# Performance work log

Hardware: AMD Instinct MI355X
Metric: run time of the kernel (lower is better)

The kernel has to match this reference:

```python
import jax, jax.numpy as jnp
import numpy as np

IN_F = 4096
OUT_F = 4096

def setup_inputs() -> dict:
    key = jax.random.key(0)
    k1, k2 = jax.random.split(key)
    x = jax.random.normal(k1, (4, 2048, IN_F), dtype=jnp.float32)
    W = jax.random.normal(k2, (OUT_F, IN_F), dtype=jnp.float32) * (1.0 / np.sqrt(IN_F))
    return {"x": x, "W": W}

def reference(x, W):
    # per-tensor scale = mean |W|, clamped
    scale = jnp.maximum(jnp.mean(jnp.abs(W)), 1e-8)
    # pentanet: 5-level quantization {-2,-1,0,1,2}
    w_quant = jnp.clip(jnp.round(W / scale), -2.0, 2.0)
    # STE: forward uses quantized weights, gradient flows to W
    w_ste = jax.lax.stop_gradient(w_quant * scale - W) + W
    # F.linear: x @ w_ste.T -> [b, s, out]
    return jnp.einsum('bsi,oi->bso', x, w_ste)
```

## Files before the change

kernel.cpp:

```cpp
#include <hip/hip_runtime.h>
#include <cstdint>
#include <cstddef>

#define IN_F 4096
#define OUT_F 4096

typedef __attribute__((ext_vector_type(8))) short bf16x8;
typedef __attribute__((ext_vector_type(4))) float f32x4;

__device__ __forceinline__ ushort f32_bf16_rne(float f) {
    uint32_t u = __builtin_bit_cast(uint32_t, f);
    uint32_t r = (u + 0x7FFFu + ((u >> 16) & 1u)) >> 16;
    return (ushort)r;
}

__device__ __forceinline__ void gload_lds16(const void* g, void* l) {
    __builtin_amdgcn_global_load_lds(
        (const __attribute__((address_space(1))) uint32_t*)g,
        (__attribute__((address_space(3))) uint32_t*)l,
        16, 0, 0);
}

__device__ __forceinline__ void bar() {
    asm volatile("s_barrier" ::: "memory");
}

__global__ void reduce_abs1(const float* __restrict__ W, float* __restrict__ part) {
    __shared__ float sm[256];
    const int b = blockIdx.x, t = threadIdx.x;
    const float* p = W + (size_t)b * 4096;
    float s = 0.f;
#pragma unroll
    for (int j = 0; j < 16; ++j) s += fabsf(p[t + 256 * j]);
    sm[t] = s;
    __syncthreads();
    for (int w = 128; w > 0; w >>= 1) {
        if (t < w) sm[t] += sm[t + w];
        __syncthreads();
    }
    if (t == 0) part[b] = sm[0];
}

__global__ void reduce_abs2(const float* __restrict__ part, float* __restrict__ scale) {
    __shared__ float sm[256];
    const int t = threadIdx.x;
    float s = 0.f;
#pragma unroll
    for (int j = 0; j < 16; ++j) s += part[t + 256 * j];
    sm[t] = s;
    __syncthreads();
    for (int w = 128; w > 0; w >>= 1) {
        if (t < w) sm[t] += sm[t + w];
        __syncthreads();
    }
    if (t == 0) {
        float m = sm[0] / 16777216.0f;
        *scale = fmaxf(m, 1e-8f);
    }
}

__global__ void quantize_w(const float* __restrict__ W, ushort* __restrict__ wq,
                           const float* __restrict__ scale_p) {
    const int i = blockIdx.x * 256 + threadIdx.x;
    const float s = *scale_p;
    float4 v = ((const float4*)W)[i];
    float q0 = fminf(fmaxf(rintf(v.x / s), -2.f), 2.f);
    float q1 = fminf(fmaxf(rintf(v.y / s), -2.f), 2.f);
    float q2 = fminf(fmaxf(rintf(v.z / s), -2.f), 2.f);
    float q3 = fminf(fmaxf(rintf(v.w / s), -2.f), 2.f);
    ushort4 o;
    o.x = f32_bf16_rne(q0); o.y = f32_bf16_rne(q1);
    o.z = f32_bf16_rne(q2); o.w = f32_bf16_rne(q3);
    ((ushort4*)wq)[i] = o;
}

__global__ void cast_x(const float* __restrict__ X, ushort* __restrict__ xh) {
    const int i = blockIdx.x * 256 + threadIdx.x;
    float4 v = ((const float4*)X)[i];
    ushort4 o;
    o.x = f32_bf16_rne(v.x); o.y = f32_bf16_rne(v.y);
    o.z = f32_bf16_rne(v.z); o.w = f32_bf16_rne(v.w);
    ((ushort4*)xh)[i] = o;
}

#define BK 64
#define BUF_BYTES 65536

__global__ __launch_bounds__(512, 2) void qgemm256(
        const ushort* __restrict__ Ab, const ushort* __restrict__ Bq,
        float* __restrict__ C, const float* __restrict__ scale_p,
        int M, int N, int K) {
    extern __shared__ __align__(16) char smem[];

    const int t = threadIdx.x;
    const int lane = t & 63;
    const int w = t >> 6;
    const int wr = w >> 2;
    const int wc = w & 3;
    const int bh = wc >> 1;

    const int MT = M >> 8;
    const int NTiles = N >> 8;
    int mt, nt;
    if (MT == 32 && NTiles == 16 && gridDim.x == 512) {
        const int x = blockIdx.x & 7;
        const int j = blockIdx.x >> 3;
        const int jr = j & 31;
        const int r = j >> 5;
        mt = (x & 3) * 8 + (jr & 7);
        nt = r * 8 + (x >> 2) * 4 + (jr >> 3);
    } else {
        const int nwg = gridDim.x;
        int wg = blockIdx.x;
        if ((nwg & 7) == 0) wg = (wg & 7) * (nwg >> 3) + (wg >> 3);
        mt = wg % MT; nt = wg / MT;
    }
    const int m0 = mt << 8;
    const int n0 = nt << 8;

    const int NT = K / BK;

    int pre[2];
#pragma unroll
    for (int ks = 0; ks < 2; ++ks)
        pre[ks] = (lane & 15) * 128 +
                  (((ks * 64) + ((lane >> 4) * 16)) ^ ((lane & 7) << 4));

    const int rowA = t >> 3;
    const int colsw = ((t & 7) ^ ((t >> 3) & 7)) << 3;
    const ushort* gA0 = Ab + (size_t)(m0 + rowA) * K + colsw;
    const ushort* gA1 = Ab + (size_t)(m0 + 128 + rowA) * K + colsw;
    const ushort* gB0 = Bq + (size_t)(n0 + rowA) * K + colsw;
    const ushort* gB1 = Bq + (size_t)(n0 + 128 + rowA) * K + colsw;
    const size_t jrow = (size_t)64 * K;
    char* lb = smem + t * 16;

    auto stA = [&](uint32_t par) {
        gload_lds16(gA0,        lb + par);
        gload_lds16(gA0 + jrow, lb + par + 8192);
        gload_lds16(gA1,        lb + par + 16384);
        gload_lds16(gA1 + jrow, lb + par + 24576);
        gA0 += 64; gA1 += 64;
    };
    auto stB = [&](uint32_t par) {
        gload_lds16(gB0,        lb + par + 32768);
        gload_lds16(gB0 + jrow, lb + par + 40960);
        gload_lds16(gB1,        lb + par + 49152);
        gload_lds16(gB1 + jrow, lb + par + 57344);
        gB0 += 64; gB1 += 64;
    };

    const char* aBbase = smem + wr * 16384;
    const char* bBbase = smem + 32768 + bh * 16384 + (wc & 1) * 8192;

    f32x4 acc[8][4];
#pragma unroll
    for (int m = 0; m < 8; ++m)
#pragma unroll
        for (int n = 0; n < 4; ++n) acc[m][n] = (f32x4){0.f, 0.f, 0.f, 0.f};

    bf16x8 a0[4][2], a1[4][2], b01[2][2], b23[2][2];

    stA(0); stB(0);
    stA(BUF_BYTES); stB(BUF_BYTES);
    asm volatile("s_waitcnt vmcnt(8)" ::: "memory");
    bar();
#pragma unroll
    for (int m = 0; m < 4; ++m)
#pragma unroll
        for (int ks = 0; ks < 2; ++ks) {
            a0[m][ks] = *(const bf16x8*)(aBbase + m * 2048 + pre[ks]);
            a1[m][ks] = *(const bf16x8*)(aBbase + (m + 4) * 2048 + pre[ks]);
        }
#pragma unroll
    for (int n = 0; n < 2; ++n)
#pragma unroll
        for (int ks = 0; ks < 2; ++ks) {
            b01[n][ks] = *(const bf16x8*)(bBbase + n * 2048 + pre[ks]);
            b23[n][ks] = *(const bf16x8*)(bBbase + (n + 2) * 2048 + pre[ks]);
        }

    for (int kt = 0; kt < NT; ++kt) {
        const uint32_t cur = (uint32_t)(kt & 1) * BUF_BYTES;
        const uint32_t nxt = cur ^ BUF_BYTES;
        const char* aBn = aBbase + nxt;
        const char* bBn = bBbase + nxt;

        asm volatile("s_waitcnt vmcnt(0)" ::: "memory");
        if (kt + 2 < NT) { stA(cur); stB(cur); }
        bar();

        __builtin_amdgcn_s_setprio(1);
#pragma unroll
        for (int m = 0; m < 4; ++m)
#pragma unroll
            for (int n = 0; n < 2; ++n)
#pragma unroll
                for (int ks = 0; ks < 2; ++ks)
                    acc[m][n] = __builtin_amdgcn_mfma_f32_16x16x32_bf16(
                        a0[m][ks], b01[n][ks], acc[m][n], 0, 0, 0);
#pragma unroll
        for (int m = 0; m < 4; ++m)
#pragma unroll
            for (int n = 0; n < 2; ++n)
#pragma unroll
                for (int ks = 0; ks < 2; ++ks)
                    acc[m + 4][n] = __builtin_amdgcn_mfma_f32_16x16x32_bf16(
                        a1[m][ks], b01[n][ks], acc[m + 4][n], 0, 0, 0);
#pragma unroll
        for (int m = 0; m < 4; ++m)
#pragma unroll
            for (int n = 0; n < 2; ++n)
#pragma unroll
                for (int ks = 0; ks < 2; ++ks)
                    acc[m][n + 2] = __builtin_amdgcn_mfma_f32_16x16x32_bf16(
                        a0[m][ks], b23[n][ks], acc[m][n + 2], 0, 0, 0);
#pragma unroll
        for (int m = 0; m < 4; ++m)
#pragma unroll
            for (int n = 0; n < 2; ++n)
#pragma unroll
                for (int ks = 0; ks < 2; ++ks)
                    acc[m + 4][n + 2] = __builtin_amdgcn_mfma_f32_16x16x32_bf16(
                        a1[m][ks], b23[n][ks], acc[m + 4][n + 2], 0, 0, 0);
        if (kt + 1 < NT) {
#pragma unroll
            for (int m = 0; m < 4; ++m)
#pragma unroll
                for (int ks = 0; ks < 2; ++ks) {
                    a0[m][ks] = *(const bf16x8*)(aBn + m * 2048 + pre[ks]);
                    a1[m][ks] = *(const bf16x8*)(aBn + (m + 4) * 2048 + pre[ks]);
                }
#pragma unroll
            for (int n = 0; n < 2; ++n)
#pragma unroll
                for (int ks = 0; ks < 2; ++ks) {
                    b01[n][ks] = *(const bf16x8*)(bBn + n * 2048 + pre[ks]);
                    b23[n][ks] = *(const bf16x8*)(bBn + (n + 2) * 2048 + pre[ks]);
                }
        }
        __builtin_amdgcn_s_setprio(0);
        asm volatile("s_waitcnt lgkmcnt(0)" ::: "memory");
        bar();
    }

    const float s = *scale_p;
#pragma unroll
    for (int m = 0; m < 8; ++m)
#pragma unroll
        for (int n = 0; n < 4; ++n) {
            const int col = n0 + wc * 64 + n * 16 + (lane & 15);
            const int rbase = m0 + wr * 128 + m * 16 + ((lane >> 4) << 2);
#pragma unroll
            for (int j = 0; j < 4; ++j)
                C[(size_t)(rbase + j) * N + col] = s * acc[m][n][j];
        }
}

template <bool ABF16>
__global__ __launch_bounds__(256) void qgemm(const void* __restrict__ Aptr,
                                             const ushort* __restrict__ Bq,
                                             float* __restrict__ C,
                                             const float* __restrict__ scale_p,
                                             int M, int N, int K) {
    __shared__ __align__(16) ushort sA[128 * 64];
    __shared__ __align__(16) ushort sB[128 * 64];

    const int t = threadIdx.x;
    const int lane = t & 63;
    const int w = t >> 6;
    const int wr = w >> 1, wc = w & 1;

    const int nwg = gridDim.x;
    int wg = blockIdx.x;
    if ((nwg & 7) == 0) wg = (wg & 7) * (nwg >> 3) + (wg >> 3);
    const int MT = M >> 7;
    const int mt = wg % MT;
    const int nt = wg / MT;
    const int m0 = mt * 128, n0 = nt * 128;

    const ushort* Ab = (const ushort*)Aptr;
    const float* Af = (const float*)Aptr;

    f32x4 zero = {0.f, 0.f, 0.f, 0.f};
    f32x4 acc[4][4];
#pragma unroll
    for (int m = 0; m < 4; ++m)
#pragma unroll
        for (int n = 0; n < 4; ++n) acc[m][n] = zero;

    for (int k0 = 0; k0 < K; k0 += 64) {
#pragma unroll
        for (int i = 0; i < 4; ++i) {
            int e = i * 2048 + t * 8;
            int r = e >> 6, c8 = (e >> 3) & 7;
            int srcc = (c8 ^ (r & 7)) * 8;
            gload_lds16(Bq + (size_t)(n0 + r) * K + (k0 + srcc), &sB[e]);
        }
        if constexpr (ABF16) {
#pragma unroll
            for (int i = 0; i < 4; ++i) {
                int e = i * 2048 + t * 8;
                int r = e >> 6, c8 = (e >> 3) & 7;
                int srcc = (c8 ^ (r & 7)) * 8;
                gload_lds16(Ab + (size_t)(m0 + r) * K + (k0 + srcc), &sA[e]);
            }
        } else {
#pragma unroll
            for (int i = 0; i < 4; ++i) {
                int e = i * 2048 + t * 8;
                int r = e >> 6, c = e & 63;
                const float* src = Af + (size_t)(m0 + r) * K + (k0 + c);
                float4 v0 = *(const float4*)src;
                float4 v1 = *(const float4*)(src + 4);
                bf16x8 pk;
                pk[0] = (short)f32_bf16_rne(v0.x); pk[1] = (short)f32_bf16_rne(v0.y);
                pk[2] = (short)f32_bf16_rne(v0.z); pk[3] = (short)f32_bf16_rne(v0.w);
                pk[4] = (short)f32_bf16_rne(v1.x); pk[5] = (short)f32_bf16_rne(v1.y);
                pk[6] = (short)f32_bf16_rne(v1.z); pk[7] = (short)f32_bf16_rne(v1.w);
                int byte = (r * 128 + c * 2) ^ ((r & 7) << 4);
                *(bf16x8*)((char*)sA + byte) = pk;
            }
        }
        __syncthreads();

#pragma unroll
        for (int ks = 0; ks < 2; ++ks) {
            const int kk = ks * 32 + ((lane >> 4) << 3);
            bf16x8 afr[4], bfr[4];
#pragma unroll
            for (int m = 0; m < 4; ++m) {
                int r = wr * 64 + m * 16 + (lane & 15);
                int byte = (r * 128 + kk * 2) ^ ((r & 7) << 4);
                afr[m] = *(const bf16x8*)((const char*)sA + byte);
            }
#pragma unroll
            for (int n = 0; n < 4; ++n) {
                int r = wc * 64 + n * 16 + (lane & 15);
                int byte = (r * 128 + kk * 2) ^ ((r & 7) << 4);
                bfr[n] = *(const bf16x8*)((const char*)sB + byte);
            }
#pragma unroll
            for (int m = 0; m < 4; ++m)
#pragma unroll
                for (int n = 0; n < 4; ++n)
                    acc[m][n] = __builtin_amdgcn_mfma_f32_16x16x32_bf16(
                        afr[m], bfr[n], acc[m][n], 0, 0, 0);
        }
        __syncthreads();
    }

    const float s = *scale_p;
#pragma unroll
    for (int m = 0; m < 4; ++m)
#pragma unroll
        for (int n = 0; n < 4; ++n) {
            const int col = n0 + wc * 64 + n * 16 + (lane & 15);
            const int rbase = m0 + wr * 64 + m * 16 + ((lane >> 4) << 2);
#pragma unroll
            for (int j = 0; j < 4; ++j)
                C[(size_t)(rbase + j) * N + col] = s * acc[m][n][j];
        }
}

__global__ void naive_qgemm(const float* __restrict__ X, const float* __restrict__ W,
                            float* __restrict__ out, const float* __restrict__ scale_p,
                            int M) {
    const int col = blockIdx.x * 256 + threadIdx.x;
    const int row = blockIdx.y;
    const float s = *scale_p;
    const float inv = 1.0f / s;
    const float* xr = X + (size_t)row * IN_F;
    const float* wrow = W + (size_t)col * IN_F;
    float acc = 0.f;
    for (int k = 0; k < IN_F; ++k) {
        float q = fminf(fmaxf(rintf(wrow[k] * inv), -2.f), 2.f);
        acc += xr[k] * q;
    }
    out[(size_t)row * OUT_F + col] = acc * s;
}

extern "C" void kernel_launch(void* const* d_in, const int* in_sizes, int n_in,
                              void* d_out, int out_size, void* d_ws, size_t ws_size,
                              hipStream_t stream) {
    const float* x = (const float*)d_in[0];
    const float* W = (const float*)d_in[1];
    float* out = (float*)d_out;
    const int M = in_sizes[0] / IN_F;
    const int K = IN_F, N = OUT_F;

    char* ws = (char*)d_ws;
    const size_t OFF_PART = 512;
    const size_t OFF_WQ = OFF_PART + 4096 * sizeof(float);
    const size_t WQ_BYTES = (size_t)N * K * sizeof(ushort);
    const size_t OFF_XH = OFF_WQ + WQ_BYTES;
    const size_t XH_BYTES = (size_t)M * K * sizeof(ushort);
    float* scale = (float*)(ws + 0);
    float* part = (float*)(ws + OFF_PART);
    ushort* wq = (ushort*)(ws + OFF_WQ);
    ushort* xh = (ushort*)(ws + OFF_XH);

    if (ws_size < OFF_WQ) return;

    reduce_abs1<<<4096, 256, 0, stream>>>(W, part);
    reduce_abs2<<<1, 256, 0, stream>>>(part, scale);

    if (ws_size >= OFF_XH + XH_BYTES && (M % 256) == 0 && (N % 256) == 0) {
        quantize_w<<<(N * K / 4) / 256, 256, 0, stream>>>(W, wq, scale);
        cast_x<<<(M * K / 4) / 256, 256, 0, stream>>>(x, xh);
        (void)hipFuncSetAttribute((const void*)qgemm256,
                                  hipFuncAttributeMaxDynamicSharedMemorySize,
                                  131072);
        qgemm256<<<(M / 256) * (N / 256), 512, 131072, stream>>>(
            xh, wq, out, scale, M, N, K);
    } else if (ws_size >= OFF_XH + XH_BYTES) {
        quantize_w<<<(N * K / 4) / 256, 256, 0, stream>>>(W, wq, scale);
        cast_x<<<(M * K / 4) / 256, 256, 0, stream>>>(x, xh);
        qgemm<true><<<(M / 128) * (N / 128), 256, 0, stream>>>(xh, wq, out, scale, M, N, K);
    } else if (ws_size >= OFF_WQ + WQ_BYTES) {
        quantize_w<<<(N * K / 4) / 256, 256, 0, stream>>>(W, wq, scale);
        qgemm<false><<<(M / 128) * (N / 128), 256, 0, stream>>>(x, wq, out, scale, M, N, K);
    } else {
        naive_qgemm<<<dim3(N / 256, M), 256, 0, stream>>>(x, W, out, scale, M);
    }
}
```

Before: 313.9 us.

## Drop register prefetch and issue one-ahead global loads per K-step

Restructures the main loop pipeline. Before, the kernel loaded two LDS stages ahead and prefetched the next tile's fragments into registers after the MFMAs. Now each iteration issues the global-to-LDS load for the next stage only, waits on the current one, then reads fragments from LDS and runs the MFMAs. This cuts register pressure and simplifies the schedule, but LDS read latency is no longer hidden behind MFMAs and global prefetch depth shrinks from two stages to one.

```diff
diff --git a/kernel.cpp b/kernel.cpp
--- a/kernel.cpp
+++ b/kernel.cpp
@@ -159,38 +159,37 @@
 #pragma unroll
         for (int n = 0; n < 4; ++n) acc[m][n] = (f32x4){0.f, 0.f, 0.f, 0.f};
 
-    bf16x8 a0[4][2], a1[4][2], b01[2][2], b23[2][2];
-
     stA(0); stB(0);
-    stA(BUF_BYTES); stB(BUF_BYTES);
-    asm volatile("s_waitcnt vmcnt(8)" ::: "memory");
-    bar();
-#pragma unroll
-    for (int m = 0; m < 4; ++m)
-#pragma unroll
-        for (int ks = 0; ks < 2; ++ks) {
-            a0[m][ks] = *(const bf16x8*)(aBbase + m * 2048 + pre[ks]);
-            a1[m][ks] = *(const bf16x8*)(aBbase + (m + 4) * 2048 + pre[ks]);
-        }
-#pragma unroll
-    for (int n = 0; n < 2; ++n)
-#pragma unroll
-        for (int ks = 0; ks < 2; ++ks) {
-            b01[n][ks] = *(const bf16x8*)(bBbase + n * 2048 + pre[ks]);
-            b23[n][ks] = *(const bf16x8*)(bBbase + (n + 2) * 2048 + pre[ks]);
-        }
 
     for (int kt = 0; kt < NT; ++kt) {
         const uint32_t cur = (uint32_t)(kt & 1) * BUF_BYTES;
-        const uint32_t nxt = cur ^ BUF_BYTES;
-        const char* aBn = aBbase + nxt;
-        const char* bBn = bBbase + nxt;
-
-        asm volatile("s_waitcnt vmcnt(0)" ::: "memory");
-        if (kt + 2 < NT) { stA(cur); stB(cur); }
+        const char* aB = aBbase + cur;
+        const char* bB = bBbase + cur;
+
+        if (kt + 1 < NT) {
+            stA(cur ^ BUF_BYTES); stB(cur ^ BUF_BYTES);
+            asm volatile("s_waitcnt vmcnt(8)" ::: "memory");
+        } else {
+            asm volatile("s_waitcnt vmcnt(0)" ::: "memory");
+        }
         bar();
 
         __builtin_amdgcn_s_setprio(1);
+        bf16x8 a0[4][2], a1[4][2], b01[2][2], b23[2][2];
+#pragma unroll
+        for (int n = 0; n < 2; ++n)
+#pragma unroll
+            for (int ks = 0; ks < 2; ++ks) {
+                b01[n][ks] = *(const bf16x8*)(bB + n * 2048 + pre[ks]);
+                b23[n][ks] = *(const bf16x8*)(bB + (n + 2) * 2048 + pre[ks]);
+            }
+#pragma unroll
+        for (int m = 0; m < 4; ++m)
+#pragma unroll
+            for (int ks = 0; ks < 2; ++ks) {
+                a0[m][ks] = *(const bf16x8*)(aB + m * 2048 + pre[ks]);
+                a1[m][ks] = *(const bf16x8*)(aB + (m + 4) * 2048 + pre[ks]);
+            }
 #pragma unroll
         for (int m = 0; m < 4; ++m)
 #pragma unroll
@@ -223,22 +222,6 @@
                 for (int ks = 0; ks < 2; ++ks)
                     acc[m + 4][n + 2] = __builtin_amdgcn_mfma_f32_16x16x32_bf16(
                         a1[m][ks], b23[n][ks], acc[m + 4][n + 2], 0, 0, 0);
-        if (kt + 1 < NT) {
-#pragma unroll
-            for (int m = 0; m < 4; ++m)
-#pragma unroll
-                for (int ks = 0; ks < 2; ++ks) {
-                    a0[m][ks] = *(const bf16x8*)(aBn + m * 2048 + pre[ks]);
-                    a1[m][ks] = *(const bf16x8*)(aBn + (m + 4) * 2048 + pre[ks]);
-                }
-#pragma unroll
-            for (int n = 0; n < 2; ++n)
-#pragma unroll
-                for (int ks = 0; ks < 2; ++ks) {
-                    b01[n][ks] = *(const bf16x8*)(bBn + n * 2048 + pre[ks]);
-                    b23[n][ks] = *(const bf16x8*)(bBn + (n + 2) * 2048 + pre[ks]);
-                }
-        }
         __builtin_amdgcn_s_setprio(0);
         asm volatile("s_waitcnt lgkmcnt(0)" ::: "memory");
         bar();
```

New measurement: 313.1 us. No clear change (-0.2%).

## Interleave LDS fragment loads with MFMA quarters and move barriers into the loop

Applied to the files above, without the earlier changes.

Restructures the GEMM main loop so LDS-to-register fragment loads (a1, b23, next b01, next a0) sit between the four MFMA quarter-blocks, with sched_barrier fences and setprio toggling. Global-to-LDS prefetch is issued after a mid-loop barrier instead of at the loop top. The aim is to hide LDS read latency behind MFMA work and cut the end-of-iteration lgkmcnt(0) plus barrier stall. The cost is more barriers per iteration and a tighter buffer-reuse ordering, which could be a correctness risk if the hazards are wrong.

```diff
diff --git a/kernel.cpp b/kernel.cpp
--- a/kernel.cpp
+++ b/kernel.cpp
@@ -19,10 +19,6 @@
         (const __attribute__((address_space(1))) uint32_t*)g,
         (__attribute__((address_space(3))) uint32_t*)l,
         16, 0, 0);
-}
-
-__device__ __forceinline__ void bar() {
-    asm volatile("s_barrier" ::: "memory");
 }
 
 __global__ void reduce_abs1(const float* __restrict__ W, float* __restrict__ part) {
@@ -135,19 +131,16 @@
     const size_t jrow = (size_t)64 * K;
     char* lb = smem + t * 16;
 
-    auto stA = [&](uint32_t par) {
+    auto st = [&](uint32_t par) {
         gload_lds16(gA0,        lb + par);
         gload_lds16(gA0 + jrow, lb + par + 8192);
         gload_lds16(gA1,        lb + par + 16384);
         gload_lds16(gA1 + jrow, lb + par + 24576);
-        gA0 += 64; gA1 += 64;
-    };
-    auto stB = [&](uint32_t par) {
         gload_lds16(gB0,        lb + par + 32768);
         gload_lds16(gB0 + jrow, lb + par + 40960);
         gload_lds16(gB1,        lb + par + 49152);
         gload_lds16(gB1 + jrow, lb + par + 57344);
-        gB0 += 64; gB1 += 64;
+        gA0 += 64; gA1 += 64; gB0 += 64; gB1 += 64;
     };
 
     const char* aBbase = smem + wr * 16384;
@@ -161,35 +154,37 @@
 
     bf16x8 a0[4][2], a1[4][2], b01[2][2], b23[2][2];
 
-    stA(0); stB(0);
-    stA(BUF_BYTES); stB(BUF_BYTES);
+    st(0);
+    st(BUF_BYTES);
     asm volatile("s_waitcnt vmcnt(8)" ::: "memory");
-    bar();
+    __builtin_amdgcn_s_barrier();
+    __builtin_amdgcn_sched_barrier(0);
+#pragma unroll
+    for (int n = 0; n < 2; ++n)
+#pragma unroll
+        for (int ks = 0; ks < 2; ++ks)
+            b01[n][ks] = *(const bf16x8*)(bBbase + n * 2048 + pre[ks]);
 #pragma unroll
     for (int m = 0; m < 4; ++m)
 #pragma unroll
-        for (int ks = 0; ks < 2; ++ks) {
+        for (int ks = 0; ks < 2; ++ks)
             a0[m][ks] = *(const bf16x8*)(aBbase + m * 2048 + pre[ks]);
-            a1[m][ks] = *(const bf16x8*)(aBbase + (m + 4) * 2048 + pre[ks]);
-        }
-#pragma unroll
-    for (int n = 0; n < 2; ++n)
-#pragma unroll
-        for (int ks = 0; ks < 2; ++ks) {
-            b01[n][ks] = *(const bf16x8*)(bBbase + n * 2048 + pre[ks]);
-            b23[n][ks] = *(const bf16x8*)(bBbase + (n + 2) * 2048 + pre[ks]);
-        }
 
     for (int kt = 0; kt < NT; ++kt) {
         const uint32_t cur = (uint32_t)(kt & 1) * BUF_BYTES;
         const uint32_t nxt = cur ^ BUF_BYTES;
+        const char* aB = aBbase + cur;
+        const char* bB = bBbase + cur;
         const char* aBn = aBbase + nxt;
         const char* bBn = bBbase + nxt;
-
-        asm volatile("s_waitcnt vmcnt(0)" ::: "memory");
-        if (kt + 2 < NT) { stA(cur); stB(cur); }
-        bar();
-
+        const bool haveNext = (kt + 1 < NT);
+
+#pragma unroll
+        for (int m = 0; m < 4; ++m)
+#pragma unroll
+            for (int ks = 0; ks < 2; ++ks)
+                a1[m][ks] = *(const bf16x8*)(aB + (m + 4) * 2048 + pre[ks]);
+        __builtin_amdgcn_sched_barrier(0);
         __builtin_amdgcn_s_setprio(1);
 #pragma unroll
         for (int m = 0; m < 4; ++m)
@@ -199,6 +194,16 @@
                 for (int ks = 0; ks < 2; ++ks)
                     acc[m][n] = __builtin_amdgcn_mfma_f32_16x16x32_bf16(
                         a0[m][ks], b01[n][ks], acc[m][n], 0, 0, 0);
+        __builtin_amdgcn_s_setprio(0);
+        __builtin_amdgcn_sched_barrier(0);
+
+#pragma unroll
+        for (int n = 0; n < 2; ++n)
+#pragma unroll
+            for (int ks = 0; ks < 2; ++ks)
+                b23[n][ks] = *(const bf16x8*)(bB + (n + 2) * 2048 + pre[ks]);
+        __builtin_amdgcn_sched_barrier(0);
+        __builtin_amdgcn_s_setprio(1);
 #pragma unroll
         for (int m = 0; m < 4; ++m)
 #pragma unroll
@@ -207,6 +212,23 @@
                 for (int ks = 0; ks < 2; ++ks)
                     acc[m + 4][n] = __builtin_amdgcn_mfma_f32_16x16x32_bf16(
                         a1[m][ks], b01[n][ks], acc[m + 4][n], 0, 0, 0);
+        __builtin_amdgcn_s_setprio(0);
+        __builtin_amdgcn_sched_barrier(0);
+        if (haveNext) {
+            asm volatile("s_waitcnt vmcnt(0)" ::: "memory");
+            __builtin_amdgcn_s_barrier();
+            __builtin_amdgcn_sched_barrier(0);
+        }
+
+        if (haveNext) {
+#pragma unroll
+            for (int n = 0; n < 2; ++n)
+#pragma unroll
+                for (int ks = 0; ks < 2; ++ks)
+                    b01[n][ks] = *(const bf16x8*)(bBn + n * 2048 + pre[ks]);
+        }
+        __builtin_amdgcn_sched_barrier(0);
+        __builtin_amdgcn_s_setprio(1);
 #pragma unroll
         for (int m = 0; m < 4; ++m)
 #pragma unroll
@@ -215,6 +237,21 @@
                 for (int ks = 0; ks < 2; ++ks)
                     acc[m][n + 2] = __builtin_amdgcn_mfma_f32_16x16x32_bf16(
                         a0[m][ks], b23[n][ks], acc[m][n + 2], 0, 0, 0);
+        __builtin_amdgcn_s_setprio(0);
+        __builtin_amdgcn_sched_barrier(0);
+
+        if (haveNext) {
+#pragma unroll
+            for (int m = 0; m < 4; ++m)
+#pragma unroll
+                for (int ks = 0; ks < 2; ++ks)
+                    a0[m][ks] = *(const bf16x8*)(aBn + m * 2048 + pre[ks]);
+        }
+        __builtin_amdgcn_sched_barrier(0);
+        __builtin_amdgcn_s_barrier();
+        __builtin_amdgcn_sched_barrier(0);
+        if (kt + 2 < NT) st(cur);
+        __builtin_amdgcn_s_setprio(1);
 #pragma unroll
         for (int m = 0; m < 4; ++m)
 #pragma unroll
@@ -223,25 +260,8 @@
                 for (int ks = 0; ks < 2; ++ks)
                     acc[m + 4][n + 2] = __builtin_amdgcn_mfma_f32_16x16x32_bf16(
                         a1[m][ks], b23[n][ks], acc[m + 4][n + 2], 0, 0, 0);
-        if (kt + 1 < NT) {
-#pragma unroll
-            for (int m = 0; m < 4; ++m)
-#pragma unroll
-                for (int ks = 0; ks < 2; ++ks) {
-                    a0[m][ks] = *(const bf16x8*)(aBn + m * 2048 + pre[ks]);
-                    a1[m][ks] = *(const bf16x8*)(aBn + (m + 4) * 2048 + pre[ks]);
-                }
-#pragma unroll
-            for (int n = 0; n < 2; ++n)
-#pragma unroll
-                for (int ks = 0; ks < 2; ++ks) {
-                    b01[n][ks] = *(const bf16x8*)(bBn + n * 2048 + pre[ks]);
-                    b23[n][ks] = *(const bf16x8*)(bBn + (n + 2) * 2048 + pre[ks]);
-                }
-        }
         __builtin_amdgcn_s_setprio(0);
-        asm volatile("s_waitcnt lgkmcnt(0)" ::: "memory");
-        bar();
+        __builtin_amdgcn_sched_barrier(0);
     }
 
     const float s = *scale_p;
```

Measured after the change: 307.4 us. 2.1% less time.
